# Kernel tuning notes

Hardware: AMD Instinct MI355X
Metric: run time of the kernel (lower is better)

Reference implementation:

```python
import jax, jax.numpy as jnp
import numpy as np

DT = 0.01


def setup_inputs() -> dict:
    key = jax.random.key(0)
    ks = jax.random.split(key, 16)
    B, T, IN, S, N, OUT, H = 512, 2048, 32, 16, 128, 8, 64
    sc = 0.1
    return {
        "obs": jax.random.normal(ks[0], (B, T, IN), jnp.float32),
        "x0": jnp.zeros((B, S), jnp.float32),
        "A_T": sc * jax.random.normal(ks[1], (S, S), jnp.float32),
        "Bw_T": sc * jax.random.normal(ks[2], (N, S), jnp.float32),
        "By_T": sc * jax.random.normal(ks[3], (IN, S), jnp.float32),
        "Cv_T": sc * jax.random.normal(ks[4], (S, N), jnp.float32),
        "Dvy_T": sc * jax.random.normal(ks[5], (IN, N), jnp.float32),
        "Cu_T": sc * jax.random.normal(ks[6], (S, OUT), jnp.float32),
        "Duw_T": sc * jax.random.normal(ks[7], (N, OUT), jnp.float32),
        "Duy_T": sc * jax.random.normal(ks[8], (IN, OUT), jnp.float32),
        "log_stds": jnp.full((OUT,), -1.6094379124341003, jnp.float32),
        "W1": sc * jax.random.normal(ks[9], (IN, H), jnp.float32),
        "b1": jnp.zeros((H,), jnp.float32),
        "W2": sc * jax.random.normal(ks[10], (H, H), jnp.float32),
        "b2": jnp.zeros((H,), jnp.float32),
        "W3": sc * jax.random.normal(ks[11], (H, 1), jnp.float32),
        "b3": jnp.zeros((1,), jnp.float32),
    }


def reference(obs, x0, A_T, Bw_T, By_T, Cv_T, Dvy_T, Cu_T, Duw_T, Duy_T,
              log_stds, W1, b1, W2, b2, W3, b3):
    B, T, _ = obs.shape

    def xdot(x, y, w=None):
        if w is None:
            w = jnp.tanh(x @ Cv_T + y @ Dvy_T)
        return x @ A_T + w @ Bw_T + y @ By_T

    def step(x, y):
        # y: [B, IN], x: [B, S]
        w = jnp.tanh(x @ Cv_T + y @ Dvy_T)          # [B, N]
        u = x @ Cu_T + w @ Duw_T + y @ Duy_T        # [B, OUT]
        k1 = xdot(x, y, w=w)
        k2 = xdot(x + DT * k1 / 2, y)
        k3 = xdot(x + DT * k2 / 2, y)
        k4 = xdot(x + DT * k3, y)
        x_next = x + DT / 6 * (k1 + 2 * k2 + 2 * k3 + k4)
        return x_next, u

    obs_t = jnp.swapaxes(obs, 0, 1)                 # [T, B, IN]
    x_final, actions_t = jax.lax.scan(step, x0, obs_t)
    actions = jnp.swapaxes(actions_t, 0, 1)         # [B, T, OUT]

    log_stds_rep = jnp.broadcast_to(log_stds, actions.shape[:2] + log_stds.shape)
    outputs = jnp.concatenate((actions, log_stds_rep), axis=2)

    # value baseline MLP over raw observations
    h = jnp.tanh(obs @ W1 + b1)
    h = jnp.tanh(h @ W2 + b2)
    value = (h @ W3 + b3).reshape(-1)               # [B*T]
    return outputs, x_final, value
```

## Files before the change

### kernel.cpp

```cpp
#include <hip/hip_runtime.h>


#define B_SZ  512
#define T_LEN 2048
#define IN_D  32
#define S_D   16
#define N_D   128
#define OUT_D 8
#define H_D   64
#define DT_C  0.01f

typedef unsigned short u16;
typedef unsigned int   u32;
typedef unsigned int uv2 __attribute__((ext_vector_type(2)));

__device__ __forceinline__ float bf2f(u16 u){ return __uint_as_float(((u32)u)<<16); }
__device__ __forceinline__ float lo2f(u32 w){ return __uint_as_float(w<<16); }
__device__ __forceinline__ float hi2f(u32 w){ return __uint_as_float(w & 0xffff0000u); }
__device__ __forceinline__ u16 f2bf(float f){
    u32 u = __float_as_uint(f);
    u32 r = (u + 0x7fffu + ((u>>16)&1u)) >> 16;
    return (u16)r;
}
__device__ __forceinline__ float fast_tanh(float a){
    float e = __builtin_amdgcn_exp2f(a * 2.8853900817779268f);
    float r = __builtin_amdgcn_rcpf(e + 1.0f);
    return fmaf(-2.0f, r, 1.0f);
}
__device__ __forceinline__ u32 getc(const uint4& v, int c){
    return c==0 ? v.x : c==1 ? v.y : c==2 ? v.z : v.w;
}

#define QUAD1 0xB1
#define QUAD2 0x4E
#define QUAD3 0x1B
#define ROR8  0x128
#define HMIR  0x141
#define RMIR  0x140
template<int CTRL>
__device__ __forceinline__ float dppf(float v){
    return __int_as_float(__builtin_amdgcn_update_dpp(
        __float_as_int(v), __float_as_int(v), CTRL, 0xF, 0xF, false));
}
__device__ __forceinline__ float pl16sum(float v){
    uv2 r = __builtin_amdgcn_permlane16_swap(__float_as_uint(v), __float_as_uint(v), false, false);
    return __uint_as_float(r[0]) + __uint_as_float(r[1]);
}
__device__ __forceinline__ float pl32sum(float v){
    uv2 r = __builtin_amdgcn_permlane32_swap(__float_as_uint(v), __float_as_uint(v), false, false);
    return __uint_as_float(r[0]) + __uint_as_float(r[1]);
}

__device__ __forceinline__ int sig4(int d){ return (d&3) ^ ((d&4)?7:0) ^ (d&8); }
__device__ __forceinline__ int sig3(int d){ return (d&3) ^ ((d&4)?7:0); }

template<bool BF16>
__device__ __forceinline__ float ldw(const void* p, int i){
    if (BF16) return bf2f(((const u16*)p)[i]);
    else      return ((const float*)p)[i];
}
template<bool BF16>
__device__ __forceinline__ float yelem(const uint4* yr, int j){
    if (BF16) { u32 w = getc(yr[j>>3], (j>>1)&3); return (j&1) ? hi2f(w) : lo2f(w); }
    else      { return __uint_as_float(getc(yr[j>>2], j&3)); }
}
template<bool BF16>
__device__ __forceinline__ void ldrow(uint4* r, const void* obs, size_t row){
    const uint4* p = (const uint4*)((const char*)obs + row * (size_t)(IN_D * (BF16 ? 2 : 4)));
    #pragma unroll
    for (int q = 0; q < (BF16 ? 4 : 8); ++q) r[q] = p[q];
}
template<bool BF16>
__device__ __forceinline__ void stout(void* out, size_t i, float v){
    if (BF16) ((u16*)out)[i] = f2bf(v);
    else      ((float*)out)[i] = v;
}

template<bool BF16>
__global__ __launch_bounds__(128, 1)
void rnn_fused(const void* __restrict__ obs,  const void* __restrict__ x0,
               const void* __restrict__ A_T,  const void* __restrict__ Bw_T,
               const void* __restrict__ By_T, const void* __restrict__ Cv_T,
               const void* __restrict__ Dvy_T,const void* __restrict__ Cu_T,
               const void* __restrict__ Duw_T,const void* __restrict__ Duy_T,
               const void* __restrict__ log_stds,
               const void* __restrict__ W1, const void* __restrict__ b1,
               const void* __restrict__ W2, const void* __restrict__ b2,
               const void* __restrict__ W3, const void* __restrict__ b3,
               void* __restrict__ out)
{
    {
        u32 w0 = *(const u32*)log_stds;
        bool is_bf16 = ((w0 & 0xffffu) == 0xBFCEu);
        if (is_bf16 != BF16) return;
    }

    const int b = blockIdx.x;
    const int t = threadIdx.x;
    const int l = t & 63;
    constexpr int NW = BF16 ? 4 : 8;

    __shared__ __align__(16) float vh[2][64];

    const size_t XF_OFF  = (size_t)B_SZ * T_LEN * 16;
    const size_t VAL_OFF = XF_OFF + (size_t)B_SZ * S_D;

    if (t < 64) {
        const int cx = l & 15;
        const int o8 = l & 7;
        const int n0 = l, n1 = l + 64;

        float Cv0x[16], Cv1x[16], AxCol[16], CuCol[16];
        #pragma unroll
        for (int m = 0; m < 16; ++m) {
            int s = cx ^ m;
            Cv0x[m] = ldw<BF16>(Cv_T, s * N_D + n0);
            Cv1x[m] = ldw<BF16>(Cv_T, s * N_D + n1);
            AxCol[m] = ldw<BF16>(A_T,  s * S_D + cx);
            CuCol[m] = ldw<BF16>(Cu_T, s * OUT_D + o8);
        }
        float Bw0x[16], Bw1x[16];
        #pragma unroll
        for (int d = 0; d < 16; ++d) {
            int s = cx ^ sig4(d);
            Bw0x[d] = ldw<BF16>(Bw_T, n0 * S_D + s);
            Bw1x[d] = ldw<BF16>(Bw_T, n1 * S_D + s);
        }
        float Duw0x[8], Duw1x[8];
        #pragma unroll
        for (int d = 0; d < 8; ++d) {
            int o = o8 ^ sig3(d);
            Duw0x[d] = ldw<BF16>(Duw_T, n0 * OUT_D + o);
            Duw1x[d] = ldw<BF16>(Duw_T, n1 * OUT_D + o);
        }
        float Dvy0[32], Dvy1[32], ByCol[32], DuyCol[32];
        #pragma unroll
        for (int j = 0; j < 32; ++j) {
            Dvy0[j]   = ldw<BF16>(Dvy_T, j * N_D + n0);
            Dvy1[j]   = ldw<BF16>(Dvy_T, j * N_D + n1);
            ByCol[j]  = ldw<BF16>(By_T,  j * S_D + cx);
            DuyCol[j] = ldw<BF16>(Duy_T, j * OUT_D + o8);
        }
        const float lsv = ldw<BF16>(log_stds, o8);

        float xb = ldw<BF16>(x0, b * S_D + cx);
        float g[16];
        #pragma unroll
        for (int m = 0; m < 16; ++m) g[m] = ldw<BF16>(x0, b * S_D + (cx ^ m));

        uint4 yr[NW];
        ldrow<BF16>(yr, obs, (size_t)b * T_LEN);

        for (int step = 0; step < T_LEN; ++step) {
            float yD0a=0.f, yD0b=0.f, yD1a=0.f, yD1b=0.f;
            float yXa=0.f, yXb=0.f, yUa=0.f, yUb=0.f;
            #pragma unroll
            for (int j = 0; j < 16; ++j) {
                float ya = yelem<BF16>(yr, j), yb2 = yelem<BF16>(yr, j + 16);
                yD0a = fmaf(ya,  Dvy0[j],     yD0a);
                yD0b = fmaf(yb2, Dvy0[j+16],  yD0b);
                yD1a = fmaf(ya,  Dvy1[j],     yD1a);
                yD1b = fmaf(yb2, Dvy1[j+16],  yD1b);
                yXa  = fmaf(ya,  ByCol[j],    yXa);
                yXb  = fmaf(yb2, ByCol[j+16], yXb);
                yUa  = fmaf(ya,  DuyCol[j],   yUa);
                yUb  = fmaf(yb2, DuyCol[j+16],yUb);
            }
            const float yD0 = yD0a + yD0b, yD1 = yD1a + yD1b;
            const float yX  = yXa + yXb,   yU  = yUa + yUb;
            {
                int nxt = (step + 1 < T_LEN) ? (step + 1) : (T_LEN - 1);
                ldrow<BF16>(yr, obs, (size_t)b * T_LEN + nxt);
            }

            float kacc = 0.f;
            #pragma unroll
            for (int i = 0; i < 4; ++i) {
                float a0a = yD0, a0b = 0.f, a1a = yD1, a1b = 0.f;
                #pragma unroll
                for (int m = 0; m < 8; ++m) {
                    a0a = fmaf(g[m],   Cv0x[m],   a0a);
                    a0b = fmaf(g[m+8], Cv0x[m+8], a0b);
                    a1a = fmaf(g[m],   Cv1x[m],   a1a);
                    a1b = fmaf(g[m+8], Cv1x[m+8], a1b);
                }
                float w0 = fast_tanh(a0a + a0b);
                float w1 = fast_tanh(a1a + a1b);

                float axAa = yX, axAb = 0.f;
                #pragma unroll
                for (int m = 0; m < 8; ++m) {
                    axAa = fmaf(g[m],   AxCol[m],   axAa);
                    axAb = fmaf(g[m+8], AxCol[m+8], axAb);
                }
                float axA = axAa + axAb;

                float pk[16];
                #pragma unroll
                for (int d = 0; d < 16; ++d) pk[d] = fmaf(w1, Bw1x[d], w0 * Bw0x[d]);
                #pragma unroll
                for (int d = 0; d < 16; d += 2) pk[d] += dppf<QUAD1>(pk[d+1]);
                #pragma unroll
                for (int d = 0; d < 16; d += 4) pk[d] += dppf<QUAD2>(pk[d+2]);
                pk[0] += dppf<HMIR>(pk[4]);
                pk[8] += dppf<HMIR>(pk[12]);
                float krow  = pk[0] + dppf<ROR8>(pk[8]);
                float kfull = pl32sum(pl16sum(krow)) + axA;

                if (i == 0) {
                    float axCua = yU, axCub = 0.f;
                    #pragma unroll
                    for (int m = 0; m < 8; ++m) {
                        axCua = fmaf(g[m],   CuCol[m],   axCua);
                        axCub = fmaf(g[m+8], CuCol[m+8], axCub);
                    }
                    float pu[8];
                    #pragma unroll
                    for (int d = 0; d < 8; ++d) pu[d] = fmaf(w1, Duw1x[d], w0 * Duw0x[d]);
                    #pragma unroll
                    for (int d = 0; d < 8; d += 2) pu[d] += dppf<QUAD1>(pu[d+1]);
                    pu[0] += dppf<QUAD2>(pu[2]);
                    pu[4] += dppf<QUAD2>(pu[6]);
                    float urow = pu[0] + dppf<HMIR>(pu[4]);
                    urow += dppf<ROR8>(urow);
                    float uo = pl32sum(pl16sum(urow)) + (axCua + axCub);
                    if (l < 16) {
                        size_t ob = ((size_t)b * T_LEN + step) * 16;
                        stout<BF16>(out, ob + l, (l < 8) ? uo : lsv);
                    }
                }

                kacc += ((i == 1 || i == 2) ? 2.0f : 1.0f) * kfull;
                float xnew;
                if (i == 0 || i == 1) xnew = fmaf(0.5f * DT_C, kfull, xb);
                else if (i == 2)      xnew = fmaf(DT_C, kfull, xb);
                else { xb = fmaf(DT_C * (1.0f / 6.0f), kacc, xb); xnew = xb; }

                g[0]  = xnew;
                g[1]  = dppf<QUAD1>(g[0]);
                g[2]  = dppf<QUAD2>(g[0]);
                g[3]  = dppf<QUAD3>(g[0]);
                g[7]  = dppf<HMIR>(g[0]);
                g[6]  = dppf<QUAD1>(g[7]);
                g[5]  = dppf<QUAD2>(g[7]);
                g[4]  = dppf<QUAD3>(g[7]);
                g[8]  = dppf<ROR8>(g[0]);
                g[9]  = dppf<QUAD1>(g[8]);
                g[10] = dppf<QUAD2>(g[8]);
                g[11] = dppf<QUAD3>(g[8]);
                g[15] = dppf<RMIR>(g[0]);
                g[14] = dppf<QUAD1>(g[15]);
                g[13] = dppf<QUAD2>(g[15]);
                g[12] = dppf<QUAD3>(g[15]);
            }
        }
        if (l < 16) {
            stout<BF16>(out, XF_OFF + (size_t)b * S_D + l, xb);
        }
    } else {
        float W1c[32], W2c[64];
        #pragma unroll
        for (int j = 0; j < 32; ++j) W1c[j] = ldw<BF16>(W1, j * H_D + l);
        #pragma unroll
        for (int j = 0; j < 64; ++j) W2c[j] = ldw<BF16>(W2, j * H_D + l);
        float b1l = ldw<BF16>(b1, l);
        float b2l = ldw<BF16>(b2, l);
        float w3l = ldw<BF16>(W3, l);
        float b3f = ldw<BF16>(b3, 0);

        uint4 yr[NW];
        ldrow<BF16>(yr, obs, (size_t)b * T_LEN);

        for (int step = 0; step < T_LEN; ++step) {
            uint4 yc[NW];
            #pragma unroll
            for (int q = 0; q < NW; ++q) yc[q] = yr[q];
            {
                int nxt = (step + 1 < T_LEN) ? (step + 1) : (T_LEN - 1);
                ldrow<BF16>(yr, obs, (size_t)b * T_LEN + nxt);
            }
            float* vhb = vh[step & 1];

            float h1a = b1l, h1b = 0.f;
            #pragma unroll
            for (int j = 0; j < 16; ++j) {
                h1a = fmaf(yelem<BF16>(yc, j),      W1c[j],    h1a);
                h1b = fmaf(yelem<BF16>(yc, j + 16), W1c[j+16], h1b);
            }
            float h1 = fast_tanh(h1a + h1b);
            vhb[l] = h1;

            float hv[64];
            #pragma unroll
            for (int q = 0; q < 16; ++q) {
                float4 v = ((const float4*)vhb)[q];
                hv[q*4+0] = v.x; hv[q*4+1] = v.y;
                hv[q*4+2] = v.z; hv[q*4+3] = v.w;
            }
            float h2a = b2l, h2b = 0.f, h2c = 0.f, h2d = 0.f;
            #pragma unroll
            for (int j = 0; j < 16; ++j) {
                h2a = fmaf(hv[j],    W2c[j],    h2a);
                h2b = fmaf(hv[j+16], W2c[j+16], h2b);
                h2c = fmaf(hv[j+32], W2c[j+32], h2c);
                h2d = fmaf(hv[j+48], W2c[j+48], h2d);
            }
            float h2 = fast_tanh((h2a + h2b) + (h2c + h2d));
            float v = h2 * w3l;
            v += __shfl_xor(v, 1);
            v += __shfl_xor(v, 2);
            v += __shfl_xor(v, 4);
            v += __shfl_xor(v, 8);
            v += __shfl_xor(v, 16);
            v += __shfl_xor(v, 32);
            if (l == 0) {
                size_t row = (size_t)b * T_LEN + step;
                stout<BF16>(out, VAL_OFF + row, v + b3f);
            }
        }
    }
}

extern "C" void kernel_launch(void* const* d_in, const int* in_sizes, int n_in,
                              void* d_out, int out_size, void* d_ws, size_t ws_size,
                              hipStream_t stream) {
    (void)in_sizes; (void)n_in; (void)out_size; (void)d_ws; (void)ws_size;
    rnn_fused<true><<<dim3(B_SZ), dim3(128), 0, stream>>>(
        d_in[0], d_in[1], d_in[2], d_in[3], d_in[4], d_in[5], d_in[6], d_in[7],
        d_in[8], d_in[9], d_in[10], d_in[11], d_in[12], d_in[13], d_in[14],
        d_in[15], d_in[16], d_out);
    rnn_fused<false><<<dim3(B_SZ), dim3(128), 0, stream>>>(
        d_in[0], d_in[1], d_in[2], d_in[3], d_in[4], d_in[5], d_in[6], d_in[7],
        d_in[8], d_in[9], d_in[10], d_in[11], d_in[12], d_in[13], d_in[14],
        d_in[15], d_in[16], d_out);
}
```

Baseline: 3.569 ms.

## Pin weights in VGPRs, widen FMA accumulator chains, use DPP for value reduction

Adds empty inline-asm register pins to every preloaded weight so the compiler keeps them in VGPRs rather than rematerialising or reloading them inside the time loop. It splits the Cv and A dot products over four accumulators instead of two to shorten the serial FMA dependency chains on the recurrent critical path. It also replaces the six shfl_xor reductions in the value MLP with DPP and permlane sums, which avoids LDS-based bpermute traffic. The pins raise register pressure and could cause spills.

Measured after the change: 3.673 ms. 2.9% more time.

```diff
diff --git a/kernel.cpp b/kernel.cpp
--- a/kernel.cpp
+++ b/kernel.cpp
@@ -13,6 +13,8 @@
 typedef unsigned short u16;
 typedef unsigned int   u32;
 typedef unsigned int uv2 __attribute__((ext_vector_type(2)));
+
+#define PIN(x) asm volatile("" : "+v"(x))
 
 __device__ __forceinline__ float bf2f(u16 u){ return __uint_as_float(((u32)u)<<16); }
 __device__ __forceinline__ float lo2f(u32 w){ return __uint_as_float(w<<16); }
@@ -114,34 +116,34 @@
         #pragma unroll
         for (int m = 0; m < 16; ++m) {
             int s = cx ^ m;
-            Cv0x[m] = ldw<BF16>(Cv_T, s * N_D + n0);
-            Cv1x[m] = ldw<BF16>(Cv_T, s * N_D + n1);
-            AxCol[m] = ldw<BF16>(A_T,  s * S_D + cx);
-            CuCol[m] = ldw<BF16>(Cu_T, s * OUT_D + o8);
+            Cv0x[m] = ldw<BF16>(Cv_T, s * N_D + n0);   PIN(Cv0x[m]);
+            Cv1x[m] = ldw<BF16>(Cv_T, s * N_D + n1);   PIN(Cv1x[m]);
+            AxCol[m] = ldw<BF16>(A_T,  s * S_D + cx);  PIN(AxCol[m]);
+            CuCol[m] = ldw<BF16>(Cu_T, s * OUT_D + o8);PIN(CuCol[m]);
         }
         float Bw0x[16], Bw1x[16];
         #pragma unroll
         for (int d = 0; d < 16; ++d) {
             int s = cx ^ sig4(d);
-            Bw0x[d] = ldw<BF16>(Bw_T, n0 * S_D + s);
-            Bw1x[d] = ldw<BF16>(Bw_T, n1 * S_D + s);
+            Bw0x[d] = ldw<BF16>(Bw_T, n0 * S_D + s);   PIN(Bw0x[d]);
+            Bw1x[d] = ldw<BF16>(Bw_T, n1 * S_D + s);   PIN(Bw1x[d]);
         }
         float Duw0x[8], Duw1x[8];
         #pragma unroll
         for (int d = 0; d < 8; ++d) {
             int o = o8 ^ sig3(d);
-            Duw0x[d] = ldw<BF16>(Duw_T, n0 * OUT_D + o);
-            Duw1x[d] = ldw<BF16>(Duw_T, n1 * OUT_D + o);
+            Duw0x[d] = ldw<BF16>(Duw_T, n0 * OUT_D + o); PIN(Duw0x[d]);
+            Duw1x[d] = ldw<BF16>(Duw_T, n1 * OUT_D + o); PIN(Duw1x[d]);
         }
         float Dvy0[32], Dvy1[32], ByCol[32], DuyCol[32];
         #pragma unroll
         for (int j = 0; j < 32; ++j) {
-            Dvy0[j]   = ldw<BF16>(Dvy_T, j * N_D + n0);
-            Dvy1[j]   = ldw<BF16>(Dvy_T, j * N_D + n1);
-            ByCol[j]  = ldw<BF16>(By_T,  j * S_D + cx);
-            DuyCol[j] = ldw<BF16>(Duy_T, j * OUT_D + o8);
-        }
-        const float lsv = ldw<BF16>(log_stds, o8);
+            Dvy0[j]   = ldw<BF16>(Dvy_T, j * N_D + n0);   PIN(Dvy0[j]);
+            Dvy1[j]   = ldw<BF16>(Dvy_T, j * N_D + n1);   PIN(Dvy1[j]);
+            ByCol[j]  = ldw<BF16>(By_T,  j * S_D + cx);   PIN(ByCol[j]);
+            DuyCol[j] = ldw<BF16>(Duy_T, j * OUT_D + o8); PIN(DuyCol[j]);
+        }
+        float lsv = ldw<BF16>(log_stds, o8); PIN(lsv);
 
         float xb = ldw<BF16>(x0, b * S_D + cx);
         float g[16];
@@ -176,24 +178,31 @@
             float kacc = 0.f;
             #pragma unroll
             for (int i = 0; i < 4; ++i) {
-                float a0a = yD0, a0b = 0.f, a1a = yD1, a1b = 0.f;
-                #pragma unroll
-                for (int m = 0; m < 8; ++m) {
-                    a0a = fmaf(g[m],   Cv0x[m],   a0a);
-                    a0b = fmaf(g[m+8], Cv0x[m+8], a0b);
-                    a1a = fmaf(g[m],   Cv1x[m],   a1a);
-                    a1b = fmaf(g[m+8], Cv1x[m+8], a1b);
+                float a0a = yD0, a0b = 0.f, a0c = 0.f, a0d = 0.f;
+                float a1a = yD1, a1b = 0.f, a1c = 0.f, a1d = 0.f;
+                #pragma unroll
+                for (int m = 0; m < 4; ++m) {
+                    a0a = fmaf(g[m],    Cv0x[m],    a0a);
+                    a0b = fmaf(g[m+4],  Cv0x[m+4],  a0b);
+                    a0c = fmaf(g[m+8],  Cv0x[m+8],  a0c);
+                    a0d = fmaf(g[m+12], Cv0x[m+12], a0d);
+                    a1a = fmaf(g[m],    Cv1x[m],    a1a);
+                    a1b = fmaf(g[m+4],  Cv1x[m+4],  a1b);
+                    a1c = fmaf(g[m+8],  Cv1x[m+8],  a1c);
+                    a1d = fmaf(g[m+12], Cv1x[m+12], a1d);
                 }
-                float w0 = fast_tanh(a0a + a0b);
-                float w1 = fast_tanh(a1a + a1b);
-
-                float axAa = yX, axAb = 0.f;
-                #pragma unroll
-                for (int m = 0; m < 8; ++m) {
-                    axAa = fmaf(g[m],   AxCol[m],   axAa);
-                    axAb = fmaf(g[m+8], AxCol[m+8], axAb);
+                float w0 = fast_tanh((a0a + a0b) + (a0c + a0d));
+                float w1 = fast_tanh((a1a + a1b) + (a1c + a1d));
+
+                float axAa = yX, axAb = 0.f, axAc = 0.f, axAd = 0.f;
+                #pragma unroll
+                for (int m = 0; m < 4; ++m) {
+                    axAa = fmaf(g[m],    AxCol[m],    axAa);
+                    axAb = fmaf(g[m+4],  AxCol[m+4],  axAb);
+                    axAc = fmaf(g[m+8],  AxCol[m+8],  axAc);
+                    axAd = fmaf(g[m+12], AxCol[m+12], axAd);
                 }
-                float axA = axAa + axAb;
+                float axA = (axAa + axAb) + (axAc + axAd);
 
                 float pk[16];
                 #pragma unroll
@@ -260,13 +269,13 @@
     } else {
         float W1c[32], W2c[64];
         #pragma unroll
-        for (int j = 0; j < 32; ++j) W1c[j] = ldw<BF16>(W1, j * H_D + l);
-        #pragma unroll
-        for (int j = 0; j < 64; ++j) W2c[j] = ldw<BF16>(W2, j * H_D + l);
-        float b1l = ldw<BF16>(b1, l);
-        float b2l = ldw<BF16>(b2, l);
-        float w3l = ldw<BF16>(W3, l);
-        float b3f = ldw<BF16>(b3, 0);
+        for (int j = 0; j < 32; ++j) { W1c[j] = ldw<BF16>(W1, j * H_D + l); PIN(W1c[j]); }
+        #pragma unroll
+        for (int j = 0; j < 64; ++j) { W2c[j] = ldw<BF16>(W2, j * H_D + l); PIN(W2c[j]); }
+        float b1l = ldw<BF16>(b1, l); PIN(b1l);
+        float b2l = ldw<BF16>(b2, l); PIN(b2l);
+        float w3l = ldw<BF16>(W3, l); PIN(w3l);
+        float b3f = ldw<BF16>(b3, 0); PIN(b3f);
 
         uint4 yr[NW];
         ldrow<BF16>(yr, obs, (size_t)b * T_LEN);
@@ -307,12 +316,11 @@
             }
             float h2 = fast_tanh((h2a + h2b) + (h2c + h2d));
             float v = h2 * w3l;
-            v += __shfl_xor(v, 1);
-            v += __shfl_xor(v, 2);
-            v += __shfl_xor(v, 4);
-            v += __shfl_xor(v, 8);
-            v += __shfl_xor(v, 16);
-            v += __shfl_xor(v, 32);
+            v += dppf<QUAD1>(v);
+            v += dppf<QUAD2>(v);
+            v += dppf<HMIR>(v);
+            v += dppf<ROR8>(v);
+            v = pl32sum(pl16sum(v));
             if (l == 0) {
                 size_t row = (size_t)b * T_LEN + step;
                 stout<BF16>(out, VAL_OFF + row, v + b3f);
```
